# Optimization experiments

Measured on AMD Instinct MI355X. Metric: run time of the kernel, lower is better.

The kernel has to match this reference:

```python
import jax, jax.numpy as jnp
import numpy as np

N = 50000   # nodes
D = 128     # input_dim
E = 1600000 # edges
K = 100     # out_nodes


def setup_inputs() -> dict:
    key = jax.random.key(0)
    ks = jax.random.split(key, 9)
    x = jax.random.normal(ks[0], (N, D), dtype=jnp.float32)
    edge_index = jax.random.randint(ks[1], (2, E), 0, N, dtype=jnp.int64)
    # PyG GCNConv params: Linear(in,out,bias=False) weight + separate bias
    s = 1.0 / np.sqrt(D)
    W1 = jax.random.uniform(ks[2], (D, D), jnp.float32, -s, s)
    b1 = jnp.zeros((D,), jnp.float32)
    W2 = jax.random.uniform(ks[3], (D, D), jnp.float32, -s, s)
    b2 = jnp.zeros((D,), jnp.float32)
    Wa = jax.random.uniform(ks[4], (D, K), jnp.float32, -s, s)
    ba = jax.random.uniform(ks[5], (K,), jnp.float32, -s, s)
    return {"x": x, "edge_index": edge_index, "W1": W1, "b1": b1,
            "W2": W2, "b2": b2, "Wa": Wa, "ba": ba}


def _gcn_conv(x, src, dst, norm, W, b, n_nodes):
    # PyG GCNConv: h = x @ W; aggregate D^-1/2 (A+I) D^-1/2 h; add bias
    h = x @ W                                  # [N, D]
    msg = h[src] * norm[:, None]               # [E+N, D] gather + scale
    agg = jax.ops.segment_sum(msg, dst, num_segments=n_nodes)  # scatter-add
    return agg + b


def reference(x, edge_index, W1, b1, W2, b2, Wa, ba):
    n = x.shape[0]
    loop = jnp.arange(n, dtype=edge_index.dtype)
    src = jnp.concatenate([edge_index[0], loop])   # add self-loops
    dst = jnp.concatenate([edge_index[1], loop])
    deg = jnp.zeros((n,), x.dtype).at[dst].add(1.0)
    dinv = jnp.where(deg > 0, jax.lax.rsqrt(deg), 0.0)
    norm = dinv[src] * dinv[dst]                   # [E+N]

    h = _gcn_conv(x, src, dst, norm, W1, b1, n)
    h = jax.nn.relu(h)
    h = _gcn_conv(h, src, dst, norm, W2, b2, n)
    s = jax.nn.softmax(h @ Wa + ba, axis=1)        # [N, K]
    return s
```

## Files before the change

kernel.cpp:

```cpp
#include <hip/hip_runtime.h>

#define D 128
#define KOUT 100
#define CHUNK 4096

typedef __attribute__((ext_vector_type(8))) short short8;
typedef __attribute__((ext_vector_type(4))) float floatx4;

__device__ inline float bf_lo(unsigned int u) { return __uint_as_float(u << 16); }
__device__ inline float bf_hi(unsigned int u) { return __uint_as_float(u & 0xFFFF0000u); }

__device__ inline unsigned int bf_round(float a) {
    unsigned int ua = __float_as_uint(a);
    return (ua + 0x7FFFu + ((ua >> 16) & 1u)) >> 16;
}
__device__ inline unsigned int pack_bf(float a, float b) {
    return bf_round(a) | (bf_round(b) << 16);
}


__launch_bounds__(256)
__global__ void bucket_pass1(const int* __restrict__ ei, int E, int nbuck, int cap,
                             int* __restrict__ bcur, unsigned int* __restrict__ bdata) {
    __shared__ int hist[256];
    __shared__ int sc[256];
    __shared__ int pfx[256];
    __shared__ int cur[256];
    __shared__ int gbase[256];
    __shared__ unsigned int lbuf[CHUNK];
    __shared__ unsigned char bkt[CHUNK];

    int tid = threadIdx.x;
    int base = blockIdx.x * CHUNK;
    int cnt = E - base; if (cnt > CHUNK) cnt = CHUNK;

    hist[tid] = 0;
    __syncthreads();

    int src[CHUNK / 256];
    int dst[CHUNK / 256];
#pragma unroll
    for (int q = 0; q < CHUNK / 256; q++) {
        int li = tid + q * 256;
        if (li < cnt) {
            src[q] = ei[base + li];
            dst[q] = ei[E + base + li];
            atomicAdd(&hist[dst[q] >> 8], 1);
        }
    }
    __syncthreads();

    int v = hist[tid];
    sc[tid] = v;
    __syncthreads();
    for (int off = 1; off < 256; off <<= 1) {
        int t = (tid >= off) ? sc[tid - off] : 0;
        __syncthreads();
        sc[tid] += t;
        __syncthreads();
    }
    int excl = sc[tid] - v;
    pfx[tid] = excl;
    cur[tid] = excl;
    gbase[tid] = 0;
    if (tid < nbuck && v > 0) gbase[tid] = atomicAdd(&bcur[tid], v);
    __syncthreads();

#pragma unroll
    for (int q = 0; q < CHUNK / 256; q++) {
        int li = tid + q * 256;
        if (li < cnt) {
            int b = dst[q] >> 8;
            int p = atomicAdd(&cur[b], 1);
            lbuf[p] = (unsigned int)src[q] | ((unsigned int)(dst[q] & 255) << 24);
            bkt[p] = (unsigned char)b;
        }
    }
    __syncthreads();

    for (int p = tid; p < cnt; p += 256) {
        int b = bkt[p];
        bdata[(size_t)b * cap + gbase[b] + (p - pfx[b])] = lbuf[p];
    }
}


__launch_bounds__(256)
__global__ void bucket_build(const unsigned int* __restrict__ bdata, const int* __restrict__ bcur,
                             int cap, int* __restrict__ deg, float* __restrict__ dinv,
                             int* __restrict__ rowptr, int* __restrict__ csr, int n, int nbuck) {
    __shared__ int cnts[256];
    __shared__ int sc[256];
    __shared__ int cur[256];
    __shared__ int bbase;

    int b = blockIdx.x, tid = threadIdx.x;
    if (tid == 0) bbase = 0;
    cnts[tid] = 0;
    __syncthreads();

    int part = 0;
    for (int t = tid; t < b; t += 256) part += bcur[t];
#pragma unroll
    for (int off = 32; off > 0; off >>= 1) part += __shfl_down(part, off);
    if ((tid & 63) == 0 && part != 0) atomicAdd(&bbase, part);

    int cnt = bcur[b];
    const unsigned int* p = bdata + (size_t)b * cap;
    for (int e = tid; e < cnt; e += 256) atomicAdd(&cnts[p[e] >> 24], 1);
    __syncthreads();

    int v = cnts[tid];
    sc[tid] = v;
    __syncthreads();
    for (int off = 1; off < 256; off <<= 1) {
        int t = (tid >= off) ? sc[tid - off] : 0;
        __syncthreads();
        sc[tid] += t;
        __syncthreads();
    }
    int gstart = bbase + (sc[tid] - v);
    int node = b * 256 + tid;
    if (node < n) {
        deg[node] = v + 1;
        dinv[node] = rsqrtf((float)(v + 1));
        rowptr[node] = gstart;
    }
    cur[tid] = gstart;
    __syncthreads();

    for (int e = tid; e < cnt; e += 256) {
        unsigned int u = p[e];
        int pos = atomicAdd(&cur[u >> 24], 1);
        csr[pos] = (int)(u & 0xFFFFFFu);
    }
}


__global__ void prep_frag_kernel(const float* __restrict__ W1, const float* __restrict__ W2,
                                 const float* __restrict__ Wa, const float* __restrict__ ba,
                                 unsigned short* __restrict__ Wf1, unsigned short* __restrict__ Wf2,
                                 unsigned short* __restrict__ WfA, float* __restrict__ bpad,
                                 int* __restrict__ bcur,
                                 unsigned int* __restrict__ zrowA, unsigned int* __restrict__ zrowB) {
    int idx = blockIdx.x * blockDim.x + threadIdx.x;
    if (idx < 3 * 16384) {
        int m = idx / 16384;
        int e = idx & 16383;
        int j = e & 7, lane = (e >> 3) & 63, ct = (e >> 9) & 7, kt = e >> 12;
        int k = kt * 32 + (lane >> 4) * 8 + j;
        int col = ct * 16 + (lane & 15);
        float val;
        unsigned short* dst;
        if (m == 0)      { val = W1[k * 128 + col]; dst = Wf1; }
        else if (m == 1) { val = W2[k * 128 + col]; dst = Wf2; }
        else             { val = (col < KOUT) ? Wa[k * KOUT + col] : 0.f; dst = WfA; }
        dst[e] = (unsigned short)bf_round(val);
    }
    if (idx < 128) bpad[idx] = (idx < KOUT) ? ba[idx] : 0.f;
    if (idx < 256) bcur[idx] = 0;
    if (idx < 64) { zrowA[idx] = 0u; zrowB[idx] = 0u; }
}


__launch_bounds__(256)
__global__ void gemm_mfma_kernel(const void* __restrict__ Xin, const unsigned short* __restrict__ Wf,
                                 const float* __restrict__ bias, const float* __restrict__ oscale,
                                 void* __restrict__ Y, int nrows, int in_bf16, int out_mode) {
    __shared__ float lds_f[64 * 130];
    unsigned short* lds_h = (unsigned short*)lds_f;
    unsigned int* lds_u = (unsigned int*)lds_f;

    int tid = threadIdx.x;
    int w = tid >> 6, lane = tid & 63;
    int quad = lane >> 4, m16 = lane & 15;
    int r0 = blockIdx.x * 64;

    if (!in_bf16) {
        int row = tid >> 2, cg = tid & 3;
        bool valid = (r0 + row) < nrows;
        const float4* Xr = (const float4*)Xin + (size_t)(r0 + row) * 32 + cg * 8;
#pragma unroll
        for (int j = 0; j < 8; j++) {
            float4 v = valid ? Xr[j] : make_float4(0.f, 0.f, 0.f, 0.f);
            int c = cg * 32 + j * 4;
            lds_u[row * 68 + (c >> 1)]     = pack_bf(v.x, v.y);
            lds_u[row * 68 + (c >> 1) + 1] = pack_bf(v.z, v.w);
        }
        __syncthreads();
    }

    floatx4 acc[8];
#pragma unroll
    for (int ct = 0; ct < 8; ct++) acc[ct] = (floatx4){0.f, 0.f, 0.f, 0.f};

    int arow = r0 + w * 16 + m16;
    if (arow > nrows - 1) arow = nrows - 1;
    const unsigned int* Xb = (const unsigned int*)Xin;

    const short8* Wf8 = (const short8*)Wf;
#pragma unroll
    for (int kt = 0; kt < 4; kt++) {
        short8 a;
        if (in_bf16) {
            a = *(const short8*)(Xb + (size_t)arow * 64 + kt * 16 + quad * 4);
        } else {
            a = *(const short8*)(lds_h + (w * 16 + m16) * 136 + kt * 32 + quad * 8);
        }
#pragma unroll
        for (int ct = 0; ct < 8; ct++) {
            short8 b = Wf8[(kt * 8 + ct) * 64 + lane];
            acc[ct] = __builtin_amdgcn_mfma_f32_16x16x32_bf16(a, b, acc[ct], 0, 0, 0);
        }
    }

    if (out_mode == 1) {
        __syncthreads();
#pragma unroll
        for (int ct = 0; ct < 8; ct++) {
#pragma unroll
            for (int r = 0; r < 4; r++) {
                int rl = w * 16 + quad * 4 + r;
                lds_f[rl * 130 + ct * 16 + m16] = acc[ct][r];
            }
        }
        __syncthreads();
        unsigned int* Yb = (unsigned int*)Y;
        for (int r = 0; r < 16; r++) {
            int row = r0 + w * 16 + r;
            if (row < nrows) {
                float sc = oscale ? oscale[row] : 1.f;
                float lo = lds_f[(w * 16 + r) * 130 + 2 * lane] * sc;
                float hi = lds_f[(w * 16 + r) * 130 + 2 * lane + 1] * sc;
                Yb[(size_t)row * 64 + lane] = pack_bf(lo, hi);
            }
        }
    } else {
        float bb[8];
#pragma unroll
        for (int ct = 0; ct < 8; ct++) bb[ct] = bias[ct * 16 + m16];
        float* Yf = (float*)Y;
#pragma unroll
        for (int r = 0; r < 4; r++) {
            int row = r0 + w * 16 + quad * 4 + r;
            float vv[8];
            float mx = -1e30f;
#pragma unroll
            for (int ct = 0; ct < 8; ct++) {
                int col = ct * 16 + m16;
                vv[ct] = (col < KOUT) ? acc[ct][r] + bb[ct] : -1e30f;
                mx = fmaxf(mx, vv[ct]);
            }
#pragma unroll
            for (int off = 1; off < 16; off <<= 1) mx = fmaxf(mx, __shfl_xor(mx, off));
            float se = 0.f;
#pragma unroll
            for (int ct = 0; ct < 8; ct++) {
                vv[ct] = (vv[ct] > -1e29f) ? __expf(vv[ct] - mx) : 0.f;
                se += vv[ct];
            }
#pragma unroll
            for (int off = 1; off < 16; off <<= 1) se += __shfl_xor(se, off);
            float inv = 1.f / se;
            if (row < nrows) {
#pragma unroll
                for (int ct = 0; ct < 8; ct++) {
                    int col = ct * 16 + m16;
                    if (col < KOUT) Yf[(size_t)row * KOUT + col] = vv[ct] * inv;
                }
            }
        }
    }
}


__launch_bounds__(256)
__global__ void aggregate_kernel(const uint4* __restrict__ Hb4, const int* __restrict__ csr,
                                 const int* __restrict__ rowptr, const int* __restrict__ deg,
                                 const float* __restrict__ dinv, const float* __restrict__ bias,
                                 unsigned int* __restrict__ Ob, int n, int do_relu) {
    int wid = threadIdx.x >> 6, lane = threadIdx.x & 63;
    int g = lane >> 4, c = lane & 15;
    int i = blockIdx.x * 4 + wid;
    if (i >= n) return;

    float di = dinv[i];
    float acc[8];
    {
        uint4 sv = Hb4[(size_t)i * 16 + c];
        unsigned int su[4] = {sv.x, sv.y, sv.z, sv.w};
        if (g != 0) { su[0] = su[1] = su[2] = su[3] = 0u; }
#pragma unroll
        for (int t = 0; t < 4; t++) {
            acc[2 * t]     = bf_lo(su[t]);
            acc[2 * t + 1] = bf_hi(su[t]);
        }
    }

    const int* cp = csr + rowptr[i];
    int cnt = deg[i] - 1;
    for (int e = 0; e < cnt; e += 16) {
        int s[4];
        uint4 v[4];
#pragma unroll
        for (int u = 0; u < 4; u++) {
            int idx = e + u * 4 + g;
            s[u] = (idx < cnt) ? cp[idx] : n;
        }
#pragma unroll
        for (int u = 0; u < 4; u++) v[u] = Hb4[(size_t)s[u] * 16 + c];
#pragma unroll
        for (int u = 0; u < 4; u++) {
            unsigned int uu[4] = {v[u].x, v[u].y, v[u].z, v[u].w};
#pragma unroll
            for (int t = 0; t < 4; t++) {
                acc[2 * t]     += bf_lo(uu[t]);
                acc[2 * t + 1] += bf_hi(uu[t]);
            }
        }
    }

#pragma unroll
    for (int j = 0; j < 8; j++) {
        acc[j] += __shfl_xor(acc[j], 16);
        acc[j] += __shfl_xor(acc[j], 32);
    }

    float2 bb = ((const float2*)bias)[c * 4 + g];
    float fx = acc[g * 2]     * di + bb.x;
    float fy = acc[g * 2 + 1] * di + bb.y;
    if (do_relu) { fx = fmaxf(fx, 0.f); fy = fmaxf(fy, 0.f); }
    Ob[(size_t)i * 64 + c * 4 + g] = pack_bf(fx, fy);
}


extern "C" void kernel_launch(void* const* d_in, const int* in_sizes, int n_in,
                              void* d_out, int out_size, void* d_ws, size_t ws_size,
                              hipStream_t stream) {
    const float* x  = (const float*)d_in[0];
    const int*   ei = (const int*)d_in[1];
    const float* W1 = (const float*)d_in[2];
    const float* b1 = (const float*)d_in[3];
    const float* W2 = (const float*)d_in[4];
    const float* b2 = (const float*)d_in[5];
    const float* Wa = (const float*)d_in[6];
    const float* ba = (const float*)d_in[7];
    float* out = (float*)d_out;

    int N = in_sizes[0] / D;
    int E = in_sizes[1] / 2;

    int nbuck = (N + 255) >> 8;
    int cap = ((E / nbuck) + 2048 + 63) & ~63;

    char* w = (char*)d_ws;
    size_t off = 0;
    auto carve = [&](size_t bytes) -> void* {
        void* p = w + off;
        off = (off + bytes + 255) & ~(size_t)255;
        return p;
    };
    int*   deg    = (int*)carve((size_t)N * 4);
    float* dinv   = (float*)carve((size_t)N * 4);
    int*   rowptr = (int*)carve((size_t)N * 4);
    int*   bcur   = (int*)carve(256 * 4);
    unsigned int* bdata = (unsigned int*)carve((size_t)nbuck * cap * 4);
    int*   csr    = (int*)carve((size_t)E * 4);
    unsigned short* Wf1 = (unsigned short*)carve(16384 * 2);
    unsigned short* Wf2 = (unsigned short*)carve(16384 * 2);
    unsigned short* WfA = (unsigned short*)carve(16384 * 2);
    float* bpad   = (float*)carve(512);
    unsigned int* HbA = (unsigned int*)carve((size_t)(N + 1) * 64 * 4);
    unsigned int* HbB = (unsigned int*)carve((size_t)(N + 1) * 64 * 4);
    (void)ws_size; (void)n_in; (void)out_size;

    int nbNode4 = (N + 3) / 4;
    int nbGemm = (N + 63) / 64;
    int nbP1 = (E + CHUNK - 1) / CHUNK;

    prep_frag_kernel<<<192, 256, 0, stream>>>(W1, W2, Wa, ba, Wf1, Wf2, WfA, bpad,
                                              bcur, HbA + (size_t)N * 64, HbB + (size_t)N * 64);
    bucket_pass1<<<nbP1, 256, 0, stream>>>(ei, E, nbuck, cap, bcur, bdata);
    bucket_build<<<nbuck, 256, 0, stream>>>(bdata, bcur, cap, deg, dinv, rowptr, csr, N, nbuck);

    gemm_mfma_kernel<<<nbGemm, 256, 0, stream>>>(x, Wf1, nullptr, dinv, HbA, N, 0, 1);
    aggregate_kernel<<<nbNode4, 256, 0, stream>>>((const uint4*)HbA, csr, rowptr, deg, dinv, b1, HbB, N, 1);
    gemm_mfma_kernel<<<nbGemm, 256, 0, stream>>>(HbB, Wf2, nullptr, dinv, HbA, N, 1, 1);
    aggregate_kernel<<<nbNode4, 256, 0, stream>>>((const uint4*)HbA, csr, rowptr, deg, dinv, b2, HbB, N, 0);
    gemm_mfma_kernel<<<nbGemm, 256, 0, stream>>>(HbB, WfA, bpad, nullptr, out, N, 1, 2);
}
```

Before: 269.4 us.

## Fuse CSR build stages into one cooperative kernel and prefetch aggregate indices

Merges the weight-fragment prep, bucket pass and bucket build kernels into one cooperative kernel separated by grid.sync, removing two launch gaps. The deg array is dropped: rowptr gains an N+1 entry and aggregate derives each node's count from rowptr differences. The aggregate loop now loads the next group of neighbor indices while the current rows are gathered, so index loads overlap with feature loads. Risks: the cooperative launch requires all 391 blocks to be co-resident given the large LDS footprint, and grid.sync adds its own cost.

```diff
diff --git a/kernel.cpp b/kernel.cpp
--- a/kernel.cpp
+++ b/kernel.cpp
@@ -1,4 +1,7 @@
 #include <hip/hip_runtime.h>
+#include <hip/hip_cooperative_groups.h>
+
+namespace cg = cooperative_groups;
 
 #define D 128
 #define KOUT 100
@@ -20,8 +23,15 @@
 
 
 __launch_bounds__(256)
-__global__ void bucket_pass1(const int* __restrict__ ei, int E, int nbuck, int cap,
-                             int* __restrict__ bcur, unsigned int* __restrict__ bdata) {
+__global__ void csr_coop_kernel(const int* __restrict__ ei, int E, int nbuck, int cap, int nbP1,
+                                const float* __restrict__ W1, const float* __restrict__ W2,
+                                const float* __restrict__ Wa, const float* __restrict__ ba,
+                                unsigned short* __restrict__ Wf1, unsigned short* __restrict__ Wf2,
+                                unsigned short* __restrict__ WfA, float* __restrict__ bpad,
+                                int* __restrict__ bcur,
+                                unsigned int* __restrict__ zrowA, unsigned int* __restrict__ zrowB,
+                                unsigned int* __restrict__ bdata, float* __restrict__ dinv,
+                                int* __restrict__ rowptr, int* __restrict__ csr, int n) {
     __shared__ int hist[256];
     __shared__ int sc[256];
     __shared__ int pfx[256];
@@ -29,122 +39,13 @@
     __shared__ int gbase[256];
     __shared__ unsigned int lbuf[CHUNK];
     __shared__ unsigned char bkt[CHUNK];
-
-    int tid = threadIdx.x;
-    int base = blockIdx.x * CHUNK;
-    int cnt = E - base; if (cnt > CHUNK) cnt = CHUNK;
-
-    hist[tid] = 0;
-    __syncthreads();
-
-    int src[CHUNK / 256];
-    int dst[CHUNK / 256];
-#pragma unroll
-    for (int q = 0; q < CHUNK / 256; q++) {
-        int li = tid + q * 256;
-        if (li < cnt) {
-            src[q] = ei[base + li];
-            dst[q] = ei[E + base + li];
-            atomicAdd(&hist[dst[q] >> 8], 1);
-        }
-    }
-    __syncthreads();
-
-    int v = hist[tid];
-    sc[tid] = v;
-    __syncthreads();
-    for (int off = 1; off < 256; off <<= 1) {
-        int t = (tid >= off) ? sc[tid - off] : 0;
-        __syncthreads();
-        sc[tid] += t;
-        __syncthreads();
-    }
-    int excl = sc[tid] - v;
-    pfx[tid] = excl;
-    cur[tid] = excl;
-    gbase[tid] = 0;
-    if (tid < nbuck && v > 0) gbase[tid] = atomicAdd(&bcur[tid], v);
-    __syncthreads();
-
-#pragma unroll
-    for (int q = 0; q < CHUNK / 256; q++) {
-        int li = tid + q * 256;
-        if (li < cnt) {
-            int b = dst[q] >> 8;
-            int p = atomicAdd(&cur[b], 1);
-            lbuf[p] = (unsigned int)src[q] | ((unsigned int)(dst[q] & 255) << 24);
-            bkt[p] = (unsigned char)b;
-        }
-    }
-    __syncthreads();
-
-    for (int p = tid; p < cnt; p += 256) {
-        int b = bkt[p];
-        bdata[(size_t)b * cap + gbase[b] + (p - pfx[b])] = lbuf[p];
-    }
-}
-
-
-__launch_bounds__(256)
-__global__ void bucket_build(const unsigned int* __restrict__ bdata, const int* __restrict__ bcur,
-                             int cap, int* __restrict__ deg, float* __restrict__ dinv,
-                             int* __restrict__ rowptr, int* __restrict__ csr, int n, int nbuck) {
-    __shared__ int cnts[256];
-    __shared__ int sc[256];
-    __shared__ int cur[256];
     __shared__ int bbase;
 
-    int b = blockIdx.x, tid = threadIdx.x;
-    if (tid == 0) bbase = 0;
-    cnts[tid] = 0;
-    __syncthreads();
-
-    int part = 0;
-    for (int t = tid; t < b; t += 256) part += bcur[t];
-#pragma unroll
-    for (int off = 32; off > 0; off >>= 1) part += __shfl_down(part, off);
-    if ((tid & 63) == 0 && part != 0) atomicAdd(&bbase, part);
-
-    int cnt = bcur[b];
-    const unsigned int* p = bdata + (size_t)b * cap;
-    for (int e = tid; e < cnt; e += 256) atomicAdd(&cnts[p[e] >> 24], 1);
-    __syncthreads();
-
-    int v = cnts[tid];
-    sc[tid] = v;
-    __syncthreads();
-    for (int off = 1; off < 256; off <<= 1) {
-        int t = (tid >= off) ? sc[tid - off] : 0;
-        __syncthreads();
-        sc[tid] += t;
-        __syncthreads();
-    }
-    int gstart = bbase + (sc[tid] - v);
-    int node = b * 256 + tid;
-    if (node < n) {
-        deg[node] = v + 1;
-        dinv[node] = rsqrtf((float)(v + 1));
-        rowptr[node] = gstart;
-    }
-    cur[tid] = gstart;
-    __syncthreads();
-
-    for (int e = tid; e < cnt; e += 256) {
-        unsigned int u = p[e];
-        int pos = atomicAdd(&cur[u >> 24], 1);
-        csr[pos] = (int)(u & 0xFFFFFFu);
-    }
-}
-
-
-__global__ void prep_frag_kernel(const float* __restrict__ W1, const float* __restrict__ W2,
-                                 const float* __restrict__ Wa, const float* __restrict__ ba,
-                                 unsigned short* __restrict__ Wf1, unsigned short* __restrict__ Wf2,
-                                 unsigned short* __restrict__ WfA, float* __restrict__ bpad,
-                                 int* __restrict__ bcur,
-                                 unsigned int* __restrict__ zrowA, unsigned int* __restrict__ zrowB) {
-    int idx = blockIdx.x * blockDim.x + threadIdx.x;
-    if (idx < 3 * 16384) {
+    cg::grid_group grid = cg::this_grid();
+    int bid = blockIdx.x, tid = threadIdx.x;
+
+    if (bid < 192) {
+        int idx = bid * 256 + tid;
         int m = idx / 16384;
         int e = idx & 16383;
         int j = e & 7, lane = (e >> 3) & 63, ct = (e >> 9) & 7, kt = e >> 12;
@@ -156,10 +57,111 @@
         else if (m == 1) { val = W2[k * 128 + col]; dst = Wf2; }
         else             { val = (col < KOUT) ? Wa[k * KOUT + col] : 0.f; dst = WfA; }
         dst[e] = (unsigned short)bf_round(val);
-    }
-    if (idx < 128) bpad[idx] = (idx < KOUT) ? ba[idx] : 0.f;
-    if (idx < 256) bcur[idx] = 0;
-    if (idx < 64) { zrowA[idx] = 0u; zrowB[idx] = 0u; }
+    } else if (bid == 192) {
+        bcur[tid] = 0;
+        if (tid == 0) rowptr[n] = E;
+    } else if (bid == 193) {
+        if (tid < 64) { zrowA[tid] = 0u; zrowB[tid] = 0u; }
+        if (tid < 128) bpad[tid] = (tid < KOUT) ? ba[tid] : 0.f;
+    }
+    grid.sync();
+
+    if (bid < nbP1) {
+        int base = bid * CHUNK;
+        int cnt = E - base; if (cnt > CHUNK) cnt = CHUNK;
+
+        hist[tid] = 0;
+        __syncthreads();
+
+        int src[CHUNK / 256];
+        int dst[CHUNK / 256];
+#pragma unroll
+        for (int q = 0; q < CHUNK / 256; q++) {
+            int li = tid + q * 256;
+            if (li < cnt) {
+                src[q] = ei[base + li];
+                dst[q] = ei[E + base + li];
+                atomicAdd(&hist[dst[q] >> 8], 1);
+            }
+        }
+        __syncthreads();
+
+        int v = hist[tid];
+        sc[tid] = v;
+        __syncthreads();
+        for (int off = 1; off < 256; off <<= 1) {
+            int t = (tid >= off) ? sc[tid - off] : 0;
+            __syncthreads();
+            sc[tid] += t;
+            __syncthreads();
+        }
+        int excl = sc[tid] - v;
+        pfx[tid] = excl;
+        cur[tid] = excl;
+        gbase[tid] = 0;
+        if (tid < nbuck && v > 0) gbase[tid] = atomicAdd(&bcur[tid], v);
+        __syncthreads();
+
+#pragma unroll
+        for (int q = 0; q < CHUNK / 256; q++) {
+            int li = tid + q * 256;
+            if (li < cnt) {
+                int b = dst[q] >> 8;
+                int p = atomicAdd(&cur[b], 1);
+                lbuf[p] = (unsigned int)src[q] | ((unsigned int)(dst[q] & 255) << 24);
+                bkt[p] = (unsigned char)b;
+            }
+        }
+        __syncthreads();
+
+        for (int p = tid; p < cnt; p += 256) {
+            int b = bkt[p];
+            bdata[(size_t)b * cap + gbase[b] + (p - pfx[b])] = lbuf[p];
+        }
+    }
+    grid.sync();
+
+    if (bid < nbuck) {
+        int b = bid;
+        if (tid == 0) bbase = 0;
+        hist[tid] = 0;
+        __syncthreads();
+
+        int part = 0;
+        for (int t = tid; t < b; t += 256) part += bcur[t];
+#pragma unroll
+        for (int off = 32; off > 0; off >>= 1) part += __shfl_down(part, off);
+        if ((tid & 63) == 0 && part != 0) atomicAdd(&bbase, part);
+
+        int cnt = bcur[b];
+        const unsigned int* p = bdata + (size_t)b * cap;
+        for (int e = tid; e < cnt; e += 256) atomicAdd(&hist[p[e] >> 24], 1);
+        __syncthreads();
+
+        int v = hist[tid];
+        sc[tid] = v;
+        __syncthreads();
+        for (int off = 1; off < 256; off <<= 1) {
+            int t = (tid >= off) ? sc[tid - off] : 0;
+            __syncthreads();
+            sc[tid] += t;
+            __syncthreads();
+        }
+        int gstart = bbase + (sc[tid] - v);
+        int node = b * 256 + tid;
+        if (node < n) {
+            dinv[node] = rsqrtf((float)(v + 1));
+            rowptr[node] = gstart;
+        }
+        cur[tid] = gstart;
+        __syncthreads();
+
+        for (int e = tid; e < cnt; e += 256) {
+            unsigned int u = p[e];
+            int pos = atomicAdd(&cur[u >> 24], 1);
+            csr[pos] = (int)(u & 0xFFFFFFu);
+        }
+    }
 }
 
 
@@ -177,13 +179,13 @@
     int r0 = blockIdx.x * 64;
 
     if (!in_bf16) {
-        int row = tid >> 2, cg = tid & 3;
+        int row = tid >> 2, cg_ = tid & 3;
         bool valid = (r0 + row) < nrows;
-        const float4* Xr = (const float4*)Xin + (size_t)(r0 + row) * 32 + cg * 8;
+        const float4* Xr = (const float4*)Xin + (size_t)(r0 + row) * 32 + cg_ * 8;
 #pragma unroll
         for (int j = 0; j < 8; j++) {
             float4 v = valid ? Xr[j] : make_float4(0.f, 0.f, 0.f, 0.f);
-            int c = cg * 32 + j * 4;
+            int c = cg_ * 32 + j * 4;
             lds_u[row * 68 + (c >> 1)]     = pack_bf(v.x, v.y);
             lds_u[row * 68 + (c >> 1) + 1] = pack_bf(v.z, v.w);
         }
@@ -276,7 +278,7 @@
 
 __launch_bounds__(256)
 __global__ void aggregate_kernel(const uint4* __restrict__ Hb4, const int* __restrict__ csr,
-                                 const int* __restrict__ rowptr, const int* __restrict__ deg,
+                                 const int* __restrict__ rowptr,
                                  const float* __restrict__ dinv, const float* __restrict__ bias,
                                  unsigned int* __restrict__ Ob, int n, int do_relu) {
     int wid = threadIdx.x >> 6, lane = threadIdx.x & 63;
@@ -285,6 +287,10 @@
     if (i >= n) return;
 
     float di = dinv[i];
+    int start = rowptr[i];
+    int cnt = rowptr[i + 1] - start;
+    const int* cp = csr + start;
+
     float acc[8];
     {
         uint4 sv = Hb4[(size_t)i * 16 + c];
@@ -297,18 +303,22 @@
         }
     }
 
-    const int* cp = csr + rowptr[i];
-    int cnt = deg[i] - 1;
+    int s[4];
+#pragma unroll
+    for (int u = 0; u < 4; u++) {
+        int idx = u * 4 + g;
+        s[u] = (idx < cnt) ? cp[idx] : n;
+    }
     for (int e = 0; e < cnt; e += 16) {
-        int s[4];
         uint4 v[4];
 #pragma unroll
+        for (int u = 0; u < 4; u++) v[u] = Hb4[(size_t)s[u] * 16 + c];
+        int ns[4];
+#pragma unroll
         for (int u = 0; u < 4; u++) {
-            int idx = e + u * 4 + g;
-            s[u] = (idx < cnt) ? cp[idx] : n;
-        }
-#pragma unroll
-        for (int u = 0; u < 4; u++) v[u] = Hb4[(size_t)s[u] * 16 + c];
+            int idx = e + 16 + u * 4 + g;
+            ns[u] = (idx < cnt) ? cp[idx] : n;
+        }
 #pragma unroll
         for (int u = 0; u < 4; u++) {
             unsigned int uu[4] = {v[u].x, v[u].y, v[u].z, v[u].w};
@@ -318,6 +328,8 @@
                 acc[2 * t + 1] += bf_hi(uu[t]);
             }
         }
+#pragma unroll
+        for (int u = 0; u < 4; u++) s[u] = ns[u];
     }
 
 #pragma unroll
@@ -360,9 +372,8 @@
         off = (off + bytes + 255) & ~(size_t)255;
         return p;
     };
-    int*   deg    = (int*)carve((size_t)N * 4);
     float* dinv   = (float*)carve((size_t)N * 4);
-    int*   rowptr = (int*)carve((size_t)N * 4);
+    int*   rowptr = (int*)carve((size_t)(N + 1) * 4);
     int*   bcur   = (int*)carve(256 * 4);
     unsigned int* bdata = (unsigned int*)carve((size_t)nbuck * cap * 4);
     int*   csr    = (int*)carve((size_t)E * 4);
@@ -378,14 +389,26 @@
     int nbGemm = (N + 63) / 64;
     int nbP1 = (E + CHUNK - 1) / CHUNK;
 
-    prep_frag_kernel<<<192, 256, 0, stream>>>(W1, W2, Wa, ba, Wf1, Wf2, WfA, bpad,
-                                              bcur, HbA + (size_t)N * 64, HbB + (size_t)N * 64);
-    bucket_pass1<<<nbP1, 256, 0, stream>>>(ei, E, nbuck, cap, bcur, bdata);
-    bucket_build<<<nbuck, 256, 0, stream>>>(bdata, bcur, cap, deg, dinv, rowptr, csr, N, nbuck);
+    int ngrid = nbP1;
+    if (ngrid < nbuck) ngrid = nbuck;
+    if (ngrid < 194) ngrid = 194;
+
+    unsigned int* zrowA = HbA + (size_t)N * 64;
+    unsigned int* zrowB = HbB + (size_t)N * 64;
+
+    void* cargs[] = {
+        (void*)&ei, (void*)&E, (void*)&nbuck, (void*)&cap, (void*)&nbP1,
+        (void*)&W1, (void*)&W2, (void*)&Wa, (void*)&ba,
+        (void*)&Wf1, (void*)&Wf2, (void*)&WfA, (void*)&bpad,
+        (void*)&bcur, (void*)&zrowA, (void*)&zrowB,
+        (void*)&bdata, (void*)&dinv, (void*)&rowptr, (void*)&csr, (void*)&N
+    };
+    (void)hipLaunchCooperativeKernel((void*)csr_coop_kernel, dim3(ngrid), dim3(256),
+                                     cargs, 0, stream);
 
     gemm_mfma_kernel<<<nbGemm, 256, 0, stream>>>(x, Wf1, nullptr, dinv, HbA, N, 0, 1);
-    aggregate_kernel<<<nbNode4, 256, 0, stream>>>((const uint4*)HbA, csr, rowptr, deg, dinv, b1, HbB, N, 1);
+    aggregate_kernel<<<nbNode4, 256, 0, stream>>>((const uint4*)HbA, csr, rowptr, dinv, b1, HbB, N, 1);
     gemm_mfma_kernel<<<nbGemm, 256, 0, stream>>>(HbB, Wf2, nullptr, dinv, HbA, N, 1, 1);
-    aggregate_kernel<<<nbNode4, 256, 0, stream>>>((const uint4*)HbA, csr, rowptr, deg, dinv, b2, HbB, N, 0);
+    aggregate_kernel<<<nbNode4, 256, 0, stream>>>((const uint4*)HbA, csr, rowptr, dinv, b2, HbB, N, 0);
     gemm_mfma_kernel<<<nbGemm, 256, 0, stream>>>(HbB, WfA, bpad, nullptr, out, N, 1, 2);
 }
```

Measured after the change: 369.2 us. +37.1%, slower.
